# Optimization experiments

Hardware: AMD Instinct MI355X
Metric: run time of the kernel (lower is better)

The kernel has to match this reference:

```python
import jax, jax.numpy as jnp
import numpy as np

NEG = jnp.float32(-1e30)  # finite stand-in for -inf (grad-safe)
BLANK = 0


def setup_inputs() -> dict:
    key = jax.random.key(0)
    k1, k2, k3, k4 = jax.random.split(key, 4)
    B, T, V, S = 64, 1024, 128, 256
    logits = jax.random.normal(k1, (B, T, V), dtype=jnp.float32)
    log_probs = jax.nn.log_softmax(logits, axis=-1)  # valid log-probs like a model head
    log_probs_length = jax.random.randint(k2, (B,), 768, T + 1)
    text_encoded = jax.random.randint(k3, (B, S), 1, V)  # labels exclude blank=0
    text_encoded_length = jax.random.randint(k4, (B,), 64, S + 1)
    return {
        "log_probs": log_probs,
        "log_probs_length": log_probs_length,
        "text_encoded": text_encoded,
        "text_encoded_length": text_encoded_length,
    }


def _ctc_loss(log_probs, input_lengths, targets, target_lengths):
    """CTC loss, matching torch.nn.CTCLoss(blank=0, reduction='mean', zero_infinity=True)."""
    B, T, V = log_probs.shape
    S = targets.shape[1]
    L2 = 2 * S + 1  # extended label sequence: blank-interleaved

    # extended labels ext[b, s]: blank at even s, target[(s-1)//2] at odd s
    ext = jnp.full((B, L2), BLANK, dtype=targets.dtype)
    ext = ext.at[:, 1::2].set(targets)

    # gather per-step log-prob of each extended label: [B, T, L2]
    lp_ext = jnp.take_along_axis(
        log_probs, jnp.broadcast_to(ext[:, None, :], (B, T, L2)), axis=2
    )

    pos = jnp.arange(L2)
    valid_s = pos[None, :] < (2 * target_lengths[:, None] + 1)  # [B, L2]
    ext_m2 = jnp.pad(ext, ((0, 0), (2, 0)), constant_values=BLANK)[:, :-2]
    # skip transition s-2 -> s allowed only at non-blank (odd) positions with differing labels
    skip_mask = (pos[None, :] >= 2) & (pos[None, :] % 2 == 1) & (ext != ext_m2)

    alpha0 = jnp.full((B, L2), NEG, dtype=log_probs.dtype)
    alpha0 = alpha0.at[:, 0].set(lp_ext[:, 0, 0])
    alpha0 = alpha0.at[:, 1].set(jnp.where(target_lengths > 0, lp_ext[:, 0, 1], NEG))
    alpha0 = jnp.where(valid_s, alpha0, NEG)

    lp_ext_T = jnp.moveaxis(lp_ext, 1, 0)  # [T, B, L2]

    def step(alpha, x):
        lp_t, t = x
        s1 = jnp.pad(alpha, ((0, 0), (1, 0)), constant_values=NEG)[:, :-1]
        s2 = jnp.pad(alpha, ((0, 0), (2, 0)), constant_values=NEG)[:, :-2]
        a = jnp.logaddexp(alpha, s1)
        a = jnp.where(skip_mask, jnp.logaddexp(a, s2), a)
        new = jnp.where(valid_s, a + lp_t, NEG)
        # freeze alpha for samples whose input sequence has ended
        new = jnp.where((t < input_lengths)[:, None], new, alpha)
        return new, None

    alpha, _ = jax.lax.scan(step, alpha0, (lp_ext_T[1:], jnp.arange(1, T)))

    L = target_lengths
    idx1 = (2 * L)[:, None]
    idx0 = jnp.maximum(2 * L - 1, 0)[:, None]
    a_blank = jnp.take_along_axis(alpha, idx1, axis=1)[:, 0]
    a_label = jnp.take_along_axis(alpha, idx0, axis=1)[:, 0]
    ll = jnp.logaddexp(a_blank, jnp.where(L > 0, a_label, NEG))
    loss_b = -ll
    # zero_infinity: zero out infeasible alignments
    loss_b = jnp.where(loss_b > 1e29, jnp.float32(0.0), loss_b)
    # reduction='mean': divide each loss by its target length, then batch-mean
    return jnp.mean(loss_b / jnp.maximum(L, 1).astype(log_probs.dtype))


def reference(log_probs, log_probs_length, text_encoded, text_encoded_length):
    return _ctc_loss(log_probs, log_probs_length, text_encoded, text_encoded_length)
```

## Files before the change

kernel.cpp:

```cpp
#include <hip/hip_runtime.h>

constexpr int B_ = 64;
constexpr int T_ = 1024;
constexpr int V_ = 128;
constexpr int S_ = 256;
constexpr int GRING = 32;
constexpr int ROWF = 384;
constexpr int NGW = 3;
constexpr float INV_LN2 = 1.4426950408889634f;
constexpr float LN2 = 0.6931471805599453f;

#define WS_DUMPF(W, b) ((W) + 64 + (size_t)(b) * 640)
#define WS_DUMPB(W, b) ((W) + 64 + 64 * 640 + (size_t)(b) * 640)
#define WS_KARR(W)     ((int*)((W) + 64 + 2 * 64 * 640))

#define WG_SCOPE __HIP_MEMORY_SCOPE_WORKGROUP

template <int CTRL>
__device__ __forceinline__ float dpp_mov0(float x) {
    return __int_as_float(__builtin_amdgcn_update_dpp(
        0, __float_as_int(x), CTRL, 0xF, 0xF, false));
}
template <int CTRL>
__device__ __forceinline__ float dpp_max(float x) {
    const float s = __int_as_float(__builtin_amdgcn_update_dpp(
        __float_as_int(x), __float_as_int(x), CTRL, 0xF, 0xF, false));
    return fmaxf(x, s);
}

__device__ __forceinline__ void poll_eq(int* p, int want) {
    while (__hip_atomic_load(p, __ATOMIC_RELAXED, WG_SCOPE) != want)
        __builtin_amdgcn_s_sleep(1);
}

__device__ __forceinline__ int wave_rescale(float a[10], int& K) {
    float mx = a[0];
    #pragma unroll
    for (int k = 1; k < 10; ++k) mx = fmaxf(mx, a[k]);
    mx = dpp_max<0x111>(mx);
    mx = dpp_max<0x112>(mx);
    mx = dpp_max<0x114>(mx);
    mx = dpp_max<0x118>(mx);
    mx = dpp_max<0x142>(mx);
    mx = dpp_max<0x143>(mx);
    const float mall = __int_as_float(
        __builtin_amdgcn_readlane(__float_as_int(mx), 63));
    int e;
    (void)frexpf(mall, &e);
    const int ks = (mall > 0.0f) ? (124 - e) : 0;
    #pragma unroll
    for (int k = 0; k < 10; ++k) a[k] = ldexpf(a[k], ks);
    K += ks;
    return ks;
}

__global__ __launch_bounds__(256) void ctc_scan(
    const float* __restrict__ lp,
    const int* __restrict__ in_len,
    const int* __restrict__ tgt,
    const int* __restrict__ tgt_len,
    float* __restrict__ W)
{
    const int b    = blockIdx.x & 63;
    const int dir  = blockIdx.x >> 6;
    const int tid  = threadIdx.x;
    const int wid  = tid >> 6;
    const int lane = tid & 63;

    __shared__ float ring[GRING * ROWF];
    __shared__ int   tags[8];
    __shared__ int   cons;

    const int L  = tgt_len[b];
    const int Tb = in_len[b];
    const float* lpb = lp + (size_t)b * T_ * V_;
    const int* tg = tgt + b * S_;

    const int tm = (Tb - 2) >> 1;
    const int Uf = tm;
    const int Ub = Tb - 2 - tm;
    const int U  = dir ? Ub : Uf;

    if (tid == 0) cons = 0;
    if (tid < 8) tags[tid] = -1;
    __syncthreads();

    if (wid >= 1) {
        const int q = wid - 1;

        int   perm[5], oddc[5];
        float vmask[5];
        #pragma unroll
        for (int c = 0; c < 5; ++c) {
            const int j = 5 * lane + c;
            if (j < L) { const int lb = tg[j]; perm[c] = lb >> 1; oddc[c] = lb & 1; vmask[c] = 1.0f; }
            else       { perm[c] = 0; oddc[c] = 0; vmask[c] = 0.0f; }
        }

        float2 R0[4], R1[4];
        auto issue = [&](float2 (&Rb)[4], int m) {
            const int n = min(4, U - 4 * m);
            #pragma unroll
            for (int r = 0; r < 4; ++r) {
                if (r < n) {
                    const int u = 4 * m + 1 + r;
                    const int t = dir ? (Tb - 1 - u) : u;
                    Rb[r] = *(const float2*)(lpb + (size_t)t * V_ + 2 * lane);
                }
            }
        };
        auto process = [&](float2 (&Rb)[4], int m) {
            while (__hip_atomic_load(&cons, __ATOMIC_RELAXED, WG_SCOPE) < 4 * m - 28)
                __builtin_amdgcn_s_sleep(1);
            const int n = min(4, U - 4 * m);
            #pragma unroll
            for (int r = 0; r < 4; ++r) {
                if (r < n) {
                    const float e0 = __builtin_exp2f(Rb[r].x * INV_LN2);
                    const float e1 = __builtin_exp2f(Rb[r].y * INV_LN2);
                    const float b0 = __int_as_float(
                        __builtin_amdgcn_readfirstlane(__float_as_int(e0)));
                    float gv[5];
                    #pragma unroll
                    for (int c = 0; c < 5; ++c) {
                        const float lo = __shfl(e0, perm[c], 64);
                        const float hi = __shfl(e1, perm[c], 64);
                        gv[c] = vmask[c] * (oddc[c] ? hi : lo);
                    }
                    float* rb = ring + ((4 * m + r) & (GRING - 1)) * ROWF;
                    ((float2*)rb)[lane]         = make_float2(b0,    gv[0]);
                    ((float2*)(rb + 128))[lane] = make_float2(gv[1], gv[2]);
                    ((float2*)(rb + 256))[lane] = make_float2(gv[3], gv[4]);
                }
            }
            asm volatile("s_waitcnt lgkmcnt(0)" ::: "memory");
            if (lane == 0)
                __hip_atomic_store(&tags[m & 7], m, __ATOMIC_RELAXED, WG_SCOPE);
        };

        int m = q;
        if (4 * m + 1 <= U) {
            issue(R0, m);
            if (4 * (m + NGW) + 1 <= U) issue(R1, m + NGW);
            while (true) {
                process(R0, m);
                if (4 * (m + 2 * NGW) + 1 <= U) issue(R0, m + 2 * NGW);
                m += NGW;
                if (4 * m + 1 > U) break;
                process(R1, m);
                if (4 * (m + 2 * NGW) + 1 <= U) issue(R1, m + 2 * NGW);
                m += NGW;
                if (4 * m + 1 > U) break;
            }
        }
        return;
    }

    float2 S[4][12];
    auto readBlock = [&](int set, int m) {
        const int base = ((4 * m) & (GRING - 1)) * ROWF + 2 * lane;
        #pragma unroll
        for (int r = 0; r < 4; ++r)
            #pragma unroll
            for (int pl = 0; pl < 3; ++pl)
                S[set][r * 3 + pl] =
                    *(const float2*)&ring[base + r * ROWF + pl * 128];
    };

    if (dir == 0) {
        float skipf[5];
        #pragma unroll
        for (int c = 0; c < 5; ++c) {
            const int j = 5 * lane + c;
            skipf[c] = (j >= 1 && j < L && tg[j] != tg[j - 1]) ? 1.0f : 0.0f;
        }
        float a[10];
        #pragma unroll
        for (int k = 0; k < 10; ++k) a[k] = 0.0f;
        {
            const float p00 = __builtin_exp2f(lpb[0] * INV_LN2);
            const float p01 = __builtin_exp2f(lpb[tg[0]] * INV_LN2);
            if (lane == 0) { a[0] = p00; a[1] = p01; }
        }
        float u9n = 0.0f;
        int K = 0;

        auto rowCore = [&](float2 c0, float2 c1, float2 c2) {
            const float u9 = u9n;
            const float p0 = c0.x;
            a[9] = (a[9] + a[8] + skipf[4] * a[7]) * c2.y;
            u9n = dpp_mov0<0x138>(a[9]);
            a[8] = (a[8] + a[7]) * p0;
            a[7] = (a[7] + a[6] + skipf[3] * a[5]) * c2.x;
            a[6] = (a[6] + a[5]) * p0;
            a[5] = (a[5] + a[4] + skipf[2] * a[3]) * c1.y;
            a[4] = (a[4] + a[3]) * p0;
            a[3] = (a[3] + a[2] + skipf[1] * a[1]) * c1.x;
            a[2] = (a[2] + a[1]) * p0;
            a[1] = (a[1] + a[0] + skipf[0] * u9) * c0.y;
            a[0] = (a[0] + u9) * p0;
        };
        auto row4 = [&](int set) {
            #pragma unroll
            for (int r = 0; r < 4; ++r)
                rowCore(S[set][r * 3], S[set][r * 3 + 1], S[set][r * 3 + 2]);
        };
        auto body = [&](int m, int setc, int setp) {
            if (4 * (m + 2) + 1 <= Uf) {
                poll_eq(&tags[(m + 2) & 7], m + 2);
                readBlock(setp, m + 2);
            }
            row4(setc);
            if (lane == 0)
                __hip_atomic_store(&cons, 4 * m + 4, __ATOMIC_RELAXED, WG_SCOPE);
        };

        const int MB4 = (Uf / 4) & ~3;
        poll_eq(&tags[0], 0); readBlock(0, 0);
        poll_eq(&tags[1], 1); readBlock(1, 1);
        for (int mb = 0; mb < MB4; mb += 4) {
            body(mb + 0, 0, 2);
            body(mb + 1, 1, 3);
            { const int ks = wave_rescale(a, K); u9n = ldexpf(u9n, ks); }
            body(mb + 2, 2, 0);
            body(mb + 3, 3, 1);
            { const int ks = wave_rescale(a, K); u9n = ldexpf(u9n, ks); }
        }
        #pragma unroll
        for (int r = 0; r < 4; ++r)
            if (4 * MB4 + 1 + r <= Uf)
                rowCore(S[0][r * 3], S[0][r * 3 + 1], S[0][r * 3 + 2]);
        #pragma unroll
        for (int r = 0; r < 4; ++r)
            if (4 * MB4 + 5 + r <= Uf)
                rowCore(S[1][r * 3], S[1][r * 3 + 1], S[1][r * 3 + 2]);
        { const int ks = wave_rescale(a, K); u9n = ldexpf(u9n, ks); }
        for (int u = 4 * MB4 + 9; u <= Uf; ++u) {
            const int bu = (u - 1) >> 2;
            poll_eq(&tags[bu & 7], bu);
            const int base = ((u - 1) & (GRING - 1)) * ROWF + 2 * lane;
            const float2 c0 = *(const float2*)&ring[base];
            const float2 c1 = *(const float2*)&ring[base + 128];
            const float2 c2 = *(const float2*)&ring[base + 256];
            rowCore(c0, c1, c2);
        }

        float* dump = WS_DUMPF(W, b);
        #pragma unroll
        for (int k = 0; k < 10; ++k) dump[10 * lane + k] = a[k];
        if (lane == 0) WS_KARR(W)[b] = K;
    } else {
        float sB[5];
        #pragma unroll
        for (int c = 0; c < 5; ++c) {
            const int j = 5 * lane + c + 1;
            sB[c] = (j < L && tg[j] != tg[j - 1]) ? 1.0f : 0.0f;
        }
        float g[10];
        #pragma unroll
        for (int k = 0; k < 10; ++k) g[k] = 0.0f;
        {
            const float pb = __builtin_exp2f(lpb[(size_t)(Tb - 1) * V_] * INV_LN2);
            const float pl = __builtin_exp2f(lpb[(size_t)(Tb - 1) * V_ + tg[L - 1]] * INV_LN2);
            #pragma unroll
            for (int k = 0; k < 10; ++k) {
                const int s = 10 * lane + k;
                if (s == 2 * L)     g[k] = pb;
                if (s == 2 * L - 1) g[k] = pl;
            }
        }
        float d0n = dpp_mov0<0x130>(g[0]);
        float d1n = dpp_mov0<0x130>(g[1]);
        int K = 0;

        auto rowCore = [&](float2 c0, float2 c1, float2 c2) {
            const float d0 = d0n, d1 = d1n;
            const float p0 = c0.x;
            g[0] = (g[0] + g[1]) * p0;
            g[1] = (g[1] + g[2] + sB[0] * g[3]) * c0.y;
            d0n = dpp_mov0<0x130>(g[0]);
            d1n = dpp_mov0<0x130>(g[1]);
            g[2] = (g[2] + g[3]) * p0;
            g[3] = (g[3] + g[4] + sB[1] * g[5]) * c1.x;
            g[4] = (g[4] + g[5]) * p0;
            g[5] = (g[5] + g[6] + sB[2] * g[7]) * c1.y;
            g[6] = (g[6] + g[7]) * p0;
            g[7] = (g[7] + g[8] + sB[3] * g[9]) * c2.x;
            g[8] = (g[8] + g[9]) * p0;
            g[9] = (g[9] + d0 + sB[4] * d1) * c2.y;
        };
        auto row4 = [&](int set) {
            #pragma unroll
            for (int r = 0; r < 4; ++r)
                rowCore(S[set][r * 3], S[set][r * 3 + 1], S[set][r * 3 + 2]);
        };
        auto body = [&](int m, int setc, int setp) {
            if (4 * (m + 2) + 1 <= Ub) {
                poll_eq(&tags[(m + 2) & 7], m + 2);
                readBlock(setp, m + 2);
            }
            row4(setc);
            if (lane == 0)
                __hip_atomic_store(&cons, 4 * m + 4, __ATOMIC_RELAXED, WG_SCOPE);
        };

        const int MB4 = (Ub / 4) & ~3;
        poll_eq(&tags[0], 0); readBlock(0, 0);
        poll_eq(&tags[1], 1); readBlock(1, 1);
        for (int mb = 0; mb < MB4; mb += 4) {
            body(mb + 0, 0, 2);
            body(mb + 1, 1, 3);
            { const int ks = wave_rescale(g, K);
              d0n = ldexpf(d0n, ks); d1n = ldexpf(d1n, ks); }
            body(mb + 2, 2, 0);
            body(mb + 3, 3, 1);
            { const int ks = wave_rescale(g, K);
              d0n = ldexpf(d0n, ks); d1n = ldexpf(d1n, ks); }
        }
        #pragma unroll
        for (int r = 0; r < 4; ++r)
            if (4 * MB4 + 1 + r <= Ub)
                rowCore(S[0][r * 3], S[0][r * 3 + 1], S[0][r * 3 + 2]);
        #pragma unroll
        for (int r = 0; r < 4; ++r)
            if (4 * MB4 + 5 + r <= Ub)
                rowCore(S[1][r * 3], S[1][r * 3 + 1], S[1][r * 3 + 2]);
        { const int ks = wave_rescale(g, K);
          d0n = ldexpf(d0n, ks); d1n = ldexpf(d1n, ks); }
        for (int u = 4 * MB4 + 9; u <= Ub; ++u) {
            const int bu = (u - 1) >> 2;
            poll_eq(&tags[bu & 7], bu);
            const int base = ((u - 1) & (GRING - 1)) * ROWF + 2 * lane;
            const float2 c0 = *(const float2*)&ring[base];
            const float2 c1 = *(const float2*)&ring[base + 128];
            const float2 c2 = *(const float2*)&ring[base + 256];
            rowCore(c0, c1, c2);
        }

        {
            const float d0 = d0n, d1 = d1n;
            g[0] = g[0] + g[1];
            g[1] = g[1] + g[2] + sB[0] * g[3];
            g[2] = g[2] + g[3];
            g[3] = g[3] + g[4] + sB[1] * g[5];
            g[4] = g[4] + g[5];
            g[5] = g[5] + g[6] + sB[2] * g[7];
            g[6] = g[6] + g[7];
            g[7] = g[7] + g[8] + sB[3] * g[9];
            g[8] = g[8] + g[9];
            g[9] = g[9] + d0 + sB[4] * d1;
        }
        float* dump = WS_DUMPB(W, b);
        #pragma unroll
        for (int k = 0; k < 10; ++k) dump[10 * lane + k] = g[k];
        if (lane == 0) WS_KARR(W)[64 + b] = K;
    }
}

__global__ void ctc_join_kernel(const float* __restrict__ W_const,
                                const int* __restrict__ tgt_len,
                                float* __restrict__ lossArr) {
    const int b = blockIdx.x;
    const int lane = threadIdx.x;
    float* W = const_cast<float*>(W_const);
    const float* dA = WS_DUMPF(W, b);
    const float* dB = WS_DUMPB(W, b);
    double sum = 0.0;
    #pragma unroll
    for (int k = 0; k < 10; ++k)
        sum += (double)dA[10 * lane + k] * (double)dB[10 * lane + k];
    #pragma unroll
    for (int d = 1; d < 64; d <<= 1) sum += __shfl_xor(sum, d, 64);
    if (lane == 0) {
        const int L = tgt_len[b];
        const int KF = WS_KARR(W)[b];
        const int KB = WS_KARR(W)[64 + b];
        float loss = 0.0f;
        if (sum > 0.0) {
            const long long ub = __double_as_longlong(sum);
            const int ex = (int)((ub >> 52) & 2047) - 1023;
            const double f = __longlong_as_double(
                (ub & 0x000FFFFFFFFFFFFFLL) | 0x3FF0000000000000LL);
            const float ll2 = __builtin_log2f((float)f)
                            + (float)(ex - KF - KB);
            loss = -(ll2 * LN2);
            if (!(loss <= 1e29f)) loss = 0.0f;
        }
        lossArr[b] = loss / (float)L;
    }
}

__global__ void ctc_reduce_kernel(const float* __restrict__ ws, float* __restrict__ out) {
    float v = ws[threadIdx.x];
    #pragma unroll
    for (int o = 32; o > 0; o >>= 1) v += __shfl_down(v, o);
    if (threadIdx.x == 0) out[0] = v / (float)B_;
}

extern "C" void kernel_launch(void* const* d_in, const int* in_sizes, int n_in,
                              void* d_out, int out_size, void* d_ws, size_t ws_size,
                              hipStream_t stream) {
    const float* lp      = (const float*)d_in[0];
    const int*   in_len  = (const int*)d_in[1];
    const int*   tgt     = (const int*)d_in[2];
    const int*   tgt_len = (const int*)d_in[3];
    float* W   = (float*)d_ws;
    float* out = (float*)d_out;

    ctc_scan<<<2 * B_, 256, 0, stream>>>(lp, in_len, tgt, tgt_len, W);
    ctc_join_kernel<<<B_, 64, 0, stream>>>(W, tgt_len, W);
    ctc_reduce_kernel<<<1, 64, 0, stream>>>(W, out);
}
```

Baseline: 126.9 us.

## Replace producer-wave LDS ring with single-wave register-pipelined gather and scan

Drops the three producer waves, the shared-memory ring and the tag/consumer polling. A single 64-lane wave now loads rows of log-probs eight at a time into double-buffered registers, and does the exp and shuffle gather inline, one row ahead of the recurrence. This removes LDS traffic and spin-wait synchronisation from the serial critical path. In exchange, the exp and shuffle gather work now sits on the same wave as the dependent recurrence and can no longer run in parallel on other waves.

After: 187.4 us. 47.7% more time.

```diff
diff --git a/kernel.cpp b/kernel.cpp
--- a/kernel.cpp
+++ b/kernel.cpp
@@ -4,17 +4,12 @@
 constexpr int T_ = 1024;
 constexpr int V_ = 128;
 constexpr int S_ = 256;
-constexpr int GRING = 32;
-constexpr int ROWF = 384;
-constexpr int NGW = 3;
 constexpr float INV_LN2 = 1.4426950408889634f;
 constexpr float LN2 = 0.6931471805599453f;
 
 #define WS_DUMPF(W, b) ((W) + 64 + (size_t)(b) * 640)
 #define WS_DUMPB(W, b) ((W) + 64 + 64 * 640 + (size_t)(b) * 640)
 #define WS_KARR(W)     ((int*)((W) + 64 + 2 * 64 * 640))
-
-#define WG_SCOPE __HIP_MEMORY_SCOPE_WORKGROUP
 
 template <int CTRL>
 __device__ __forceinline__ float dpp_mov0(float x) {
@@ -26,11 +21,6 @@
     const float s = __int_as_float(__builtin_amdgcn_update_dpp(
         __float_as_int(x), __float_as_int(x), CTRL, 0xF, 0xF, false));
     return fmaxf(x, s);
-}
-
-__device__ __forceinline__ void poll_eq(int* p, int want) {
-    while (__hip_atomic_load(p, __ATOMIC_RELAXED, WG_SCOPE) != want)
-        __builtin_amdgcn_s_sleep(1);
 }
 
 __device__ __forceinline__ int wave_rescale(float a[10], int& K) {
@@ -54,7 +44,7 @@
     return ks;
 }
 
-__global__ __launch_bounds__(256) void ctc_scan(
+__global__ __launch_bounds__(64) void ctc_scan(
     const float* __restrict__ lp,
     const int* __restrict__ in_len,
     const int* __restrict__ tgt,
@@ -63,13 +53,7 @@
 {
     const int b    = blockIdx.x & 63;
     const int dir  = blockIdx.x >> 6;
-    const int tid  = threadIdx.x;
-    const int wid  = tid >> 6;
-    const int lane = tid & 63;
-
-    __shared__ float ring[GRING * ROWF];
-    __shared__ int   tags[8];
-    __shared__ int   cons;
+    const int lane = threadIdx.x;
 
     const int L  = tgt_len[b];
     const int Tb = in_len[b];
@@ -81,91 +65,44 @@
     const int Ub = Tb - 2 - tm;
     const int U  = dir ? Ub : Uf;
 
-    if (tid == 0) cons = 0;
-    if (tid < 8) tags[tid] = -1;
-    __syncthreads();
-
-    if (wid >= 1) {
-        const int q = wid - 1;
-
-        int   perm[5], oddc[5];
-        float vmask[5];
+    int   perm[5], oddc[5];
+    float vmask[5];
+    #pragma unroll
+    for (int c = 0; c < 5; ++c) {
+        const int j = 5 * lane + c;
+        if (j < L) { const int lb = tg[j]; perm[c] = lb >> 1; oddc[c] = lb & 1; vmask[c] = 1.0f; }
+        else       { perm[c] = 0; oddc[c] = 0; vmask[c] = 0.0f; }
+    }
+
+    auto loadRow = [&](int u) -> float2 {
+        const int t = dir ? (Tb - 1 - u) : u;
+        return *(const float2*)(lpb + (size_t)t * V_ + 2 * lane);
+    };
+    auto gather = [&](float2 Rv, float2& c0, float2& c1, float2& c2) {
+        const float e0 = __builtin_exp2f(Rv.x * INV_LN2);
+        const float e1 = __builtin_exp2f(Rv.y * INV_LN2);
+        const float p0 = __int_as_float(
+            __builtin_amdgcn_readfirstlane(__float_as_int(e0)));
+        float gv[5];
         #pragma unroll
         for (int c = 0; c < 5; ++c) {
-            const int j = 5 * lane + c;
-            if (j < L) { const int lb = tg[j]; perm[c] = lb >> 1; oddc[c] = lb & 1; vmask[c] = 1.0f; }
-            else       { perm[c] = 0; oddc[c] = 0; vmask[c] = 0.0f; }
-        }
-
-        float2 R0[4], R1[4];
-        auto issue = [&](float2 (&Rb)[4], int m) {
-            const int n = min(4, U - 4 * m);
-            #pragma unroll
-            for (int r = 0; r < 4; ++r) {
-                if (r < n) {
-                    const int u = 4 * m + 1 + r;
-                    const int t = dir ? (Tb - 1 - u) : u;
-                    Rb[r] = *(const float2*)(lpb + (size_t)t * V_ + 2 * lane);
-                }
-            }
-        };
-        auto process = [&](float2 (&Rb)[4], int m) {
-            while (__hip_atomic_load(&cons, __ATOMIC_RELAXED, WG_SCOPE) < 4 * m - 28)
-                __builtin_amdgcn_s_sleep(1);
-            const int n = min(4, U - 4 * m);
-            #pragma unroll
-            for (int r = 0; r < 4; ++r) {
-                if (r < n) {
-                    const float e0 = __builtin_exp2f(Rb[r].x * INV_LN2);
-                    const float e1 = __builtin_exp2f(Rb[r].y * INV_LN2);
-                    const float b0 = __int_as_float(
-                        __builtin_amdgcn_readfirstlane(__float_as_int(e0)));
-                    float gv[5];
-                    #pragma unroll
-                    for (int c = 0; c < 5; ++c) {
-                        const float lo = __shfl(e0, perm[c], 64);
-                        const float hi = __shfl(e1, perm[c], 64);
-                        gv[c] = vmask[c] * (oddc[c] ? hi : lo);
-                    }
-                    float* rb = ring + ((4 * m + r) & (GRING - 1)) * ROWF;
-                    ((float2*)rb)[lane]         = make_float2(b0,    gv[0]);
-                    ((float2*)(rb + 128))[lane] = make_float2(gv[1], gv[2]);
-                    ((float2*)(rb + 256))[lane] = make_float2(gv[3], gv[4]);
-                }
-            }
-            asm volatile("s_waitcnt lgkmcnt(0)" ::: "memory");
-            if (lane == 0)
-                __hip_atomic_store(&tags[m & 7], m, __ATOMIC_RELAXED, WG_SCOPE);
-        };
-
-        int m = q;
-        if (4 * m + 1 <= U) {
-            issue(R0, m);
-            if (4 * (m + NGW) + 1 <= U) issue(R1, m + NGW);
-            while (true) {
-                process(R0, m);
-                if (4 * (m + 2 * NGW) + 1 <= U) issue(R0, m + 2 * NGW);
-                m += NGW;
-                if (4 * m + 1 > U) break;
-                process(R1, m);
-                if (4 * (m + 2 * NGW) + 1 <= U) issue(R1, m + 2 * NGW);
-                m += NGW;
-                if (4 * m + 1 > U) break;
-            }
-        }
-        return;
-    }
-
-    float2 S[4][12];
-    auto readBlock = [&](int set, int m) {
-        const int base = ((4 * m) & (GRING - 1)) * ROWF + 2 * lane;
-        #pragma unroll
-        for (int r = 0; r < 4; ++r)
-            #pragma unroll
-            for (int pl = 0; pl < 3; ++pl)
-                S[set][r * 3 + pl] =
-                    *(const float2*)&ring[base + r * ROWF + pl * 128];
+            const float lo = __shfl(e0, perm[c], 64);
+            const float hi = __shfl(e1, perm[c], 64);
+            gv[c] = vmask[c] * (oddc[c] ? hi : lo);
+        }
+        c0 = make_float2(p0,    gv[0]);
+        c1 = make_float2(gv[1], gv[2]);
+        c2 = make_float2(gv[3], gv[4]);
     };
+
+    float2 RA[8], RB[8];
+    auto issueChunk = [&](float2 (&R)[8], int c) {
+        #pragma unroll
+        for (int r = 0; r < 8; ++r) R[r] = loadRow(8 * c + 1 + r);
+    };
+
+    const int nch   = U >> 3;
+    const int ntail = U & 7;
 
     if (dir == 0) {
         float skipf[5];
@@ -200,49 +137,37 @@
             a[1] = (a[1] + a[0] + skipf[0] * u9) * c0.y;
             a[0] = (a[0] + u9) * p0;
         };
-        auto row4 = [&](int set) {
-            #pragma unroll
-            for (int r = 0; r < 4; ++r)
-                rowCore(S[set][r * 3], S[set][r * 3 + 1], S[set][r * 3 + 2]);
+        auto processChunk = [&](float2 (&R)[8]) {
+            float2 c0, c1, c2, n0, n1, n2;
+            gather(R[0], c0, c1, c2);
+            #pragma unroll
+            for (int r = 0; r < 8; ++r) {
+                if (r < 7) gather(R[r + 1], n0, n1, n2);
+                rowCore(c0, c1, c2);
+                if (r < 7) { c0 = n0; c1 = n1; c2 = n2; }
+            }
+            const int ks = wave_rescale(a, K);
+            u9n = ldexpf(u9n, ks);
         };
-        auto body = [&](int m, int setc, int setp) {
-            if (4 * (m + 2) + 1 <= Uf) {
-                poll_eq(&tags[(m + 2) & 7], m + 2);
-                readBlock(setp, m + 2);
-            }
-            row4(setc);
-            if (lane == 0)
-                __hip_atomic_store(&cons, 4 * m + 4, __ATOMIC_RELAXED, WG_SCOPE);
-        };
-
-        const int MB4 = (Uf / 4) & ~3;
-        poll_eq(&tags[0], 0); readBlock(0, 0);
-        poll_eq(&tags[1], 1); readBlock(1, 1);
-        for (int mb = 0; mb < MB4; mb += 4) {
-            body(mb + 0, 0, 2);
-            body(mb + 1, 1, 3);
-            { const int ks = wave_rescale(a, K); u9n = ldexpf(u9n, ks); }
-            body(mb + 2, 2, 0);
-            body(mb + 3, 3, 1);
-            { const int ks = wave_rescale(a, K); u9n = ldexpf(u9n, ks); }
-        }
-        #pragma unroll
-        for (int r = 0; r < 4; ++r)
-            if (4 * MB4 + 1 + r <= Uf)
-                rowCore(S[0][r * 3], S[0][r * 3 + 1], S[0][r * 3 + 2]);
-        #pragma unroll
-        for (int r = 0; r < 4; ++r)
-            if (4 * MB4 + 5 + r <= Uf)
-                rowCore(S[1][r * 3], S[1][r * 3 + 1], S[1][r * 3 + 2]);
-        { const int ks = wave_rescale(a, K); u9n = ldexpf(u9n, ks); }
-        for (int u = 4 * MB4 + 9; u <= Uf; ++u) {
-            const int bu = (u - 1) >> 2;
-            poll_eq(&tags[bu & 7], bu);
-            const int base = ((u - 1) & (GRING - 1)) * ROWF + 2 * lane;
-            const float2 c0 = *(const float2*)&ring[base];
-            const float2 c1 = *(const float2*)&ring[base + 128];
-            const float2 c2 = *(const float2*)&ring[base + 256];
-            rowCore(c0, c1, c2);
+
+        issueChunk(RA, 0);
+        if (nch > 1) issueChunk(RB, 1);
+        for (int c = 0; c < nch; ++c) {
+            if ((c & 1) == 0) { processChunk(RA); if (c + 2 < nch) issueChunk(RA, c + 2); }
+            else              { processChunk(RB); if (c + 2 < nch) issueChunk(RB, c + 2); }
+        }
+        {
+            float2 RT[7];
+            #pragma unroll
+            for (int i = 0; i < 7; ++i)
+                if (i < ntail) RT[i] = loadRow(8 * nch + 1 + i);
+            #pragma unroll
+            for (int i = 0; i < 7; ++i)
+                if (i < ntail) {
+                    float2 c0, c1, c2;
+                    gather(RT[i], c0, c1, c2);
+                    rowCore(c0, c1, c2);
+                }
         }
 
         float* dump = WS_DUMPF(W, b);
@@ -289,52 +214,37 @@
             g[8] = (g[8] + g[9]) * p0;
             g[9] = (g[9] + d0 + sB[4] * d1) * c2.y;
         };
-        auto row4 = [&](int set) {
-            #pragma unroll
-            for (int r = 0; r < 4; ++r)
-                rowCore(S[set][r * 3], S[set][r * 3 + 1], S[set][r * 3 + 2]);
+        auto processChunk = [&](float2 (&R)[8]) {
+            float2 c0, c1, c2, n0, n1, n2;
+            gather(R[0], c0, c1, c2);
+            #pragma unroll
+            for (int r = 0; r < 8; ++r) {
+                if (r < 7) gather(R[r + 1], n0, n1, n2);
+                rowCore(c0, c1, c2);
+                if (r < 7) { c0 = n0; c1 = n1; c2 = n2; }
+            }
+            const int ks = wave_rescale(g, K);
+            d0n = ldexpf(d0n, ks); d1n = ldexpf(d1n, ks);
         };
-        auto body = [&](int m, int setc, int setp) {
-            if (4 * (m + 2) + 1 <= Ub) {
-                poll_eq(&tags[(m + 2) & 7], m + 2);
-                readBlock(setp, m + 2);
-            }
-            row4(setc);
-            if (lane == 0)
-                __hip_atomic_store(&cons, 4 * m + 4, __ATOMIC_RELAXED, WG_SCOPE);
-        };
-
-        const int MB4 = (Ub / 4) & ~3;
-        poll_eq(&tags[0], 0); readBlock(0, 0);
-        poll_eq(&tags[1], 1); readBlock(1, 1);
-        for (int mb = 0; mb < MB4; mb += 4) {
-            body(mb + 0, 0, 2);
-            body(mb + 1, 1, 3);
-            { const int ks = wave_rescale(g, K);
-              d0n = ldexpf(d0n, ks); d1n = ldexpf(d1n, ks); }
-            body(mb + 2, 2, 0);
-            body(mb + 3, 3, 1);
-            { const int ks = wave_rescale(g, K);
-              d0n = ldexpf(d0n, ks); d1n = ldexpf(d1n, ks); }
-        }
-        #pragma unroll
-        for (int r = 0; r < 4; ++r)
-            if (4 * MB4 + 1 + r <= Ub)
-                rowCore(S[0][r * 3], S[0][r * 3 + 1], S[0][r * 3 + 2]);
-        #pragma unroll
-        for (int r = 0; r < 4; ++r)
-            if (4 * MB4 + 5 + r <= Ub)
-                rowCore(S[1][r * 3], S[1][r * 3 + 1], S[1][r * 3 + 2]);
-        { const int ks = wave_rescale(g, K);
-          d0n = ldexpf(d0n, ks); d1n = ldexpf(d1n, ks); }
-        for (int u = 4 * MB4 + 9; u <= Ub; ++u) {
-            const int bu = (u - 1) >> 2;
-            poll_eq(&tags[bu & 7], bu);
-            const int base = ((u - 1) & (GRING - 1)) * ROWF + 2 * lane;
-            const float2 c0 = *(const float2*)&ring[base];
-            const float2 c1 = *(const float2*)&ring[base + 128];
-            const float2 c2 = *(const float2*)&ring[base + 256];
-            rowCore(c0, c1, c2);
+
+        issueChunk(RA, 0);
+        if (nch > 1) issueChunk(RB, 1);
+        for (int c = 0; c < nch; ++c) {
+            if ((c & 1) == 0) { processChunk(RA); if (c + 2 < nch) issueChunk(RA, c + 2); }
+            else              { processChunk(RB); if (c + 2 < nch) issueChunk(RB, c + 2); }
+        }
+        {
+            float2 RT[7];
+            #pragma unroll
+            for (int i = 0; i < 7; ++i)
+                if (i < ntail) RT[i] = loadRow(8 * nch + 1 + i);
+            #pragma unroll
+            for (int i = 0; i < 7; ++i)
+                if (i < ntail) {
+                    float2 c0, c1, c2;
+                    gather(RT[i], c0, c1, c2);
+                    rowCore(c0, c1, c2);
+                }
         }
 
         {
@@ -407,7 +317,7 @@
     float* W   = (float*)d_ws;
     float* out = (float*)d_out;
 
-    ctc_scan<<<2 * B_, 256, 0, stream>>>(lp, in_len, tgt, tgt_len, W);
+    ctc_scan<<<2 * B_, 64, 0, stream>>>(lp, in_len, tgt, tgt_len, W);
     ctc_join_kernel<<<B_, 64, 0, stream>>>(W, tgt_len, W);
     ctc_reduce_kernel<<<1, 64, 0, stream>>>(W, out);
 }
```

## Enlarge producer chunks to 16 rows, batch consumer reads, fuse join and reduce

Applied to the files above, without the earlier changes.

Producer waves now each prefetch and process 16 timesteps per chunk instead of 4. The LDS ring doubles to 64 rows and each row is repacked as a float4 plus a float2. The scan wave reads 8-row halves, rescales every 8 rows and publishes progress less often, cutting poll and sync overhead per step. The join and final-mean kernels are merged into one 256-thread launch to drop a kernel launch. In exchange the code uses more LDS and registers and adds more complex tail handling.

After: 143.7 us. +13.3%, slower.

```diff
diff --git a/kernel.cpp b/kernel.cpp
--- a/kernel.cpp
+++ b/kernel.cpp
@@ -4,8 +4,9 @@
 constexpr int T_ = 1024;
 constexpr int V_ = 128;
 constexpr int S_ = 256;
-constexpr int GRING = 32;
+constexpr int GRING = 64;
 constexpr int ROWF = 384;
+constexpr int NTAG = 4;
 constexpr int NGW = 3;
 constexpr float INV_LN2 = 1.4426950408889634f;
 constexpr float LN2 = 0.6931471805599453f;
@@ -15,6 +16,11 @@
 #define WS_KARR(W)     ((int*)((W) + 64 + 2 * 64 * 640))
 
 #define WG_SCOPE __HIP_MEMORY_SCOPE_WORKGROUP
+
+__device__ __forceinline__ void poll_eq(int* p, int want) {
+    while (__hip_atomic_load(p, __ATOMIC_RELAXED, WG_SCOPE) != want)
+        __builtin_amdgcn_s_sleep(1);
+}
 
 template <int CTRL>
 __device__ __forceinline__ float dpp_mov0(float x) {
@@ -26,11 +32,6 @@
     const float s = __int_as_float(__builtin_amdgcn_update_dpp(
         __float_as_int(x), __float_as_int(x), CTRL, 0xF, 0xF, false));
     return fmaxf(x, s);
-}
-
-__device__ __forceinline__ void poll_eq(int* p, int want) {
-    while (__hip_atomic_load(p, __ATOMIC_RELAXED, WG_SCOPE) != want)
-        __builtin_amdgcn_s_sleep(1);
 }
 
 __device__ __forceinline__ int wave_rescale(float a[10], int& K) {
@@ -68,7 +69,7 @@
     const int lane = tid & 63;
 
     __shared__ float ring[GRING * ROWF];
-    __shared__ int   tags[8];
+    __shared__ int   tags[NTAG];
     __shared__ int   cons;
 
     const int L  = tgt_len[b];
@@ -82,7 +83,7 @@
     const int U  = dir ? Ub : Uf;
 
     if (tid == 0) cons = 0;
-    if (tid < 8) tags[tid] = -1;
+    if (tid < NTAG) tags[tid] = -1;
     __syncthreads();
 
     if (wid >= 1) {
@@ -97,28 +98,27 @@
             else       { perm[c] = 0; oddc[c] = 0; vmask[c] = 0.0f; }
         }
 
-        float2 R0[4], R1[4];
-        auto issue = [&](float2 (&Rb)[4], int m) {
-            const int n = min(4, U - 4 * m);
-            #pragma unroll
-            for (int r = 0; r < 4; ++r) {
-                if (r < n) {
-                    const int u = 4 * m + 1 + r;
+        float2 R0[16], R1[16];
+        auto issue = [&](float2 (&R)[16], int h) {
+            #pragma unroll
+            for (int i = 0; i < 16; ++i) {
+                const int u = 16 * h + 1 + i;
+                if (u <= U) {
                     const int t = dir ? (Tb - 1 - u) : u;
-                    Rb[r] = *(const float2*)(lpb + (size_t)t * V_ + 2 * lane);
+                    R[i] = *(const float2*)(lpb + (size_t)t * V_ + 2 * lane);
                 }
             }
         };
-        auto process = [&](float2 (&Rb)[4], int m) {
-            while (__hip_atomic_load(&cons, __ATOMIC_RELAXED, WG_SCOPE) < 4 * m - 28)
+        auto process = [&](float2 (&R)[16], int h) {
+            while (__hip_atomic_load(&cons, __ATOMIC_RELAXED, WG_SCOPE) < 16 * h - 48)
                 __builtin_amdgcn_s_sleep(1);
-            const int n = min(4, U - 4 * m);
-            #pragma unroll
-            for (int r = 0; r < 4; ++r) {
-                if (r < n) {
-                    const float e0 = __builtin_exp2f(Rb[r].x * INV_LN2);
-                    const float e1 = __builtin_exp2f(Rb[r].y * INV_LN2);
-                    const float b0 = __int_as_float(
+            #pragma unroll
+            for (int i = 0; i < 16; ++i) {
+                const int u = 16 * h + 1 + i;
+                if (u <= U) {
+                    const float e0 = __builtin_exp2f(R[i].x * INV_LN2);
+                    const float e1 = __builtin_exp2f(R[i].y * INV_LN2);
+                    const float p0 = __int_as_float(
                         __builtin_amdgcn_readfirstlane(__float_as_int(e0)));
                     float gv[5];
                     #pragma unroll
@@ -127,45 +127,55 @@
                         const float hi = __shfl(e1, perm[c], 64);
                         gv[c] = vmask[c] * (oddc[c] ? hi : lo);
                     }
-                    float* rb = ring + ((4 * m + r) & (GRING - 1)) * ROWF;
-                    ((float2*)rb)[lane]         = make_float2(b0,    gv[0]);
-                    ((float2*)(rb + 128))[lane] = make_float2(gv[1], gv[2]);
-                    ((float2*)(rb + 256))[lane] = make_float2(gv[3], gv[4]);
+                    float* rb = ring + ((u - 1) & (GRING - 1)) * ROWF;
+                    *(float4*)&rb[4 * lane] = make_float4(p0, gv[0], gv[1], gv[2]);
+                    *(float2*)&rb[256 + 2 * lane] = make_float2(gv[3], gv[4]);
                 }
             }
             asm volatile("s_waitcnt lgkmcnt(0)" ::: "memory");
             if (lane == 0)
-                __hip_atomic_store(&tags[m & 7], m, __ATOMIC_RELAXED, WG_SCOPE);
+                __hip_atomic_store(&tags[h & (NTAG - 1)], h, __ATOMIC_RELAXED, WG_SCOPE);
         };
 
         int m = q;
-        if (4 * m + 1 <= U) {
+        if (16 * m + 1 <= U) {
             issue(R0, m);
-            if (4 * (m + NGW) + 1 <= U) issue(R1, m + NGW);
+            if (16 * (m + NGW) + 1 <= U) issue(R1, m + NGW);
             while (true) {
                 process(R0, m);
-                if (4 * (m + 2 * NGW) + 1 <= U) issue(R0, m + 2 * NGW);
+                if (16 * (m + 2 * NGW) + 1 <= U) issue(R0, m + 2 * NGW);
                 m += NGW;
-                if (4 * m + 1 > U) break;
+                if (16 * m + 1 > U) break;
                 process(R1, m);
-                if (4 * (m + 2 * NGW) + 1 <= U) issue(R1, m + 2 * NGW);
+                if (16 * (m + 2 * NGW) + 1 <= U) issue(R1, m + 2 * NGW);
                 m += NGW;
-                if (4 * m + 1 > U) break;
+                if (16 * m + 1 > U) break;
             }
         }
         return;
     }
 
-    float2 S[4][12];
-    auto readBlock = [&](int set, int m) {
-        const int base = ((4 * m) & (GRING - 1)) * ROWF + 2 * lane;
-        #pragma unroll
-        for (int r = 0; r < 4; ++r)
-            #pragma unroll
-            for (int pl = 0; pl < 3; ++pl)
-                S[set][r * 3 + pl] =
-                    *(const float2*)&ring[base + r * ROWF + pl * 128];
+    float4 A4[8], B4[8];
+    float2 A2[8], B2[8];
+    auto readHalfA = [&](int j) {
+        const int base = ((8 * j) & (GRING - 1)) * ROWF;
+        #pragma unroll
+        for (int r = 0; r < 8; ++r) {
+            A4[r] = *(const float4*)&ring[base + r * ROWF + 4 * lane];
+            A2[r] = *(const float2*)&ring[base + r * ROWF + 256 + 2 * lane];
+        }
     };
+    auto readHalfB = [&](int j) {
+        const int base = ((8 * j) & (GRING - 1)) * ROWF;
+        #pragma unroll
+        for (int r = 0; r < 8; ++r) {
+            B4[r] = *(const float4*)&ring[base + r * ROWF + 4 * lane];
+            B2[r] = *(const float2*)&ring[base + r * ROWF + 256 + 2 * lane];
+        }
+    };
+
+    const int NHfull = U >> 3;
+    const int lastH  = (U - 1) >> 3;
 
     if (dir == 0) {
         float skipf[5];
@@ -200,49 +210,57 @@
             a[1] = (a[1] + a[0] + skipf[0] * u9) * c0.y;
             a[0] = (a[0] + u9) * p0;
         };
-        auto row4 = [&](int set) {
-            #pragma unroll
-            for (int r = 0; r < 4; ++r)
-                rowCore(S[set][r * 3], S[set][r * 3 + 1], S[set][r * 3 + 2]);
-        };
-        auto body = [&](int m, int setc, int setp) {
-            if (4 * (m + 2) + 1 <= Uf) {
-                poll_eq(&tags[(m + 2) & 7], m + 2);
-                readBlock(setp, m + 2);
-            }
-            row4(setc);
+        auto consume8A = [&]() {
+            #pragma unroll
+            for (int r = 0; r < 8; ++r)
+                rowCore(make_float2(A4[r].x, A4[r].y),
+                        make_float2(A4[r].z, A4[r].w), A2[r]);
+        };
+        auto consume8B = [&]() {
+            #pragma unroll
+            for (int r = 0; r < 8; ++r)
+                rowCore(make_float2(B4[r].x, B4[r].y),
+                        make_float2(B4[r].z, B4[r].w), B2[r]);
+        };
+
+        poll_eq(&tags[0], 0);
+        readHalfA(0);
+        int j = 0;
+        while (j + 2 <= NHfull) {
+            { const int H = j + 1;
+              if (H <= lastH) {
+                  if ((H & 1) == 0) poll_eq(&tags[(H >> 1) & (NTAG - 1)], H >> 1);
+                  readHalfB(H);
+              } }
+            consume8A();
+            { const int ks = wave_rescale(a, K); u9n = ldexpf(u9n, ks); }
+            { const int H = j + 2;
+              if (H <= lastH) {
+                  if ((H & 1) == 0) poll_eq(&tags[(H >> 1) & (NTAG - 1)], H >> 1);
+                  readHalfA(H);
+              } }
+            consume8B();
+            { const int ks = wave_rescale(a, K); u9n = ldexpf(u9n, ks); }
             if (lane == 0)
-                __hip_atomic_store(&cons, 4 * m + 4, __ATOMIC_RELAXED, WG_SCOPE);
-        };
-
-        const int MB4 = (Uf / 4) & ~3;
-        poll_eq(&tags[0], 0); readBlock(0, 0);
-        poll_eq(&tags[1], 1); readBlock(1, 1);
-        for (int mb = 0; mb < MB4; mb += 4) {
-            body(mb + 0, 0, 2);
-            body(mb + 1, 1, 3);
+                __hip_atomic_store(&cons, 8 * (j + 2), __ATOMIC_RELAXED, WG_SCOPE);
+            j += 2;
+        }
+        if (j < NHfull) {
+            consume8A();
             { const int ks = wave_rescale(a, K); u9n = ldexpf(u9n, ks); }
-            body(mb + 2, 2, 0);
-            body(mb + 3, 3, 1);
-            { const int ks = wave_rescale(a, K); u9n = ldexpf(u9n, ks); }
-        }
-        #pragma unroll
-        for (int r = 0; r < 4; ++r)
-            if (4 * MB4 + 1 + r <= Uf)
-                rowCore(S[0][r * 3], S[0][r * 3 + 1], S[0][r * 3 + 2]);
-        #pragma unroll
-        for (int r = 0; r < 4; ++r)
-            if (4 * MB4 + 5 + r <= Uf)
-                rowCore(S[1][r * 3], S[1][r * 3 + 1], S[1][r * 3 + 2]);
-        { const int ks = wave_rescale(a, K); u9n = ldexpf(u9n, ks); }
-        for (int u = 4 * MB4 + 9; u <= Uf; ++u) {
-            const int bu = (u - 1) >> 2;
-            poll_eq(&tags[bu & 7], bu);
-            const int base = ((u - 1) & (GRING - 1)) * ROWF + 2 * lane;
-            const float2 c0 = *(const float2*)&ring[base];
-            const float2 c1 = *(const float2*)&ring[base + 128];
-            const float2 c2 = *(const float2*)&ring[base + 256];
-            rowCore(c0, c1, c2);
+            if (lane == 0)
+                __hip_atomic_store(&cons, 8 * (j + 1), __ATOMIC_RELAXED, WG_SCOPE);
+            j++;
+        }
+        if (8 * NHfull < U) {
+            const int sb = (8 * NHfull) >> 4;
+            poll_eq(&tags[sb & (NTAG - 1)], sb);
+            for (int u = 8 * NHfull + 1; u <= U; ++u) {
+                const int base = ((u - 1) & (GRING - 1)) * ROWF;
+                const float4 v4 = *(const float4*)&ring[base + 4 * lane];
+                const float2 v2 = *(const float2*)&ring[base + 256 + 2 * lane];
+                rowCore(make_float2(v4.x, v4.y), make_float2(v4.z, v4.w), v2);
+            }
         }
 
         float* dump = WS_DUMPF(W, b);
@@ -289,52 +307,60 @@
             g[8] = (g[8] + g[9]) * p0;
             g[9] = (g[9] + d0 + sB[4] * d1) * c2.y;
         };
-        auto row4 = [&](int set) {
-            #pragma unroll
-            for (int r = 0; r < 4; ++r)
-                rowCore(S[set][r * 3], S[set][r * 3 + 1], S[set][r * 3 + 2]);
-        };
-        auto body = [&](int m, int setc, int setp) {
-            if (4 * (m + 2) + 1 <= Ub) {
-                poll_eq(&tags[(m + 2) & 7], m + 2);
-                readBlock(setp, m + 2);
-            }
-            row4(setc);
-            if (lane == 0)
-                __hip_atomic_store(&cons, 4 * m + 4, __ATOMIC_RELAXED, WG_SCOPE);
-        };
-
-        const int MB4 = (Ub / 4) & ~3;
-        poll_eq(&tags[0], 0); readBlock(0, 0);
-        poll_eq(&tags[1], 1); readBlock(1, 1);
-        for (int mb = 0; mb < MB4; mb += 4) {
-            body(mb + 0, 0, 2);
-            body(mb + 1, 1, 3);
+        auto consume8A = [&]() {
+            #pragma unroll
+            for (int r = 0; r < 8; ++r)
+                rowCore(make_float2(A4[r].x, A4[r].y),
+                        make_float2(A4[r].z, A4[r].w), A2[r]);
+        };
+        auto consume8B = [&]() {
+            #pragma unroll
+            for (int r = 0; r < 8; ++r)
+                rowCore(make_float2(B4[r].x, B4[r].y),
+                        make_float2(B4[r].z, B4[r].w), B2[r]);
+        };
+
+        poll_eq(&tags[0], 0);
+        readHalfA(0);
+        int j = 0;
+        while (j + 2 <= NHfull) {
+            { const int H = j + 1;
+              if (H <= lastH) {
+                  if ((H & 1) == 0) poll_eq(&tags[(H >> 1) & (NTAG - 1)], H >> 1);
+                  readHalfB(H);
+              } }
+            consume8A();
             { const int ks = wave_rescale(g, K);
               d0n = ldexpf(d0n, ks); d1n = ldexpf(d1n, ks); }
-            body(mb + 2, 2, 0);
-            body(mb + 3, 3, 1);
+            { const int H = j + 2;
+              if (H <= lastH) {
+                  if ((H & 1) == 0) poll_eq(&tags[(H >> 1) & (NTAG - 1)], H >> 1);
+                  readHalfA(H);
+              } }
+            consume8B();
             { const int ks = wave_rescale(g, K);
               d0n = ldexpf(d0n, ks); d1n = ldexpf(d1n, ks); }
-        }
-        #pragma unroll
-        for (int r = 0; r < 4; ++r)
-            if (4 * MB4 + 1 + r <= Ub)
-                rowCore(S[0][r * 3], S[0][r * 3 + 1], S[0][r * 3 + 2]);
-        #pragma unroll
-        for (int r = 0; r < 4; ++r)
-            if (4 * MB4 + 5 + r <= Ub)
-                rowCore(S[1][r * 3], S[1][r * 3 + 1], S[1][r * 3 + 2]);
-        { const int ks = wave_rescale(g, K);
-          d0n = ldexpf(d0n, ks); d1n = ldexpf(d1n, ks); }
-        for (int u = 4 * MB4 + 9; u <= Ub; ++u) {
-            const int bu = (u - 1) >> 2;
-            poll_eq(&tags[bu & 7], bu);
-            const int base = ((u - 1) & (GRING - 1)) * ROWF + 2 * lane;
-            const float2 c0 = *(const float2*)&ring[base];
-            const float2 c1 = *(const float2*)&ring[base + 128];
-            const float2 c2 = *(const float2*)&ring[base + 256];
-            rowCore(c0, c1, c2);
+            if (lane == 0)
+                __hip_atomic_store(&cons, 8 * (j + 2), __ATOMIC_RELAXED, WG_SCOPE);
+            j += 2;
+        }
+        if (j < NHfull) {
+            consume8A();
+            { const int ks = wave_rescale(g, K);
+              d0n = ldexpf(d0n, ks); d1n = ldexpf(d1n, ks); }
+            if (lane == 0)
+                __hip_atomic_store(&cons, 8 * (j + 1), __ATOMIC_RELAXED, WG_SCOPE);
+            j++;
+        }
+        if (8 * NHfull < U) {
+            const int sb = (8 * NHfull) >> 4;
+            poll_eq(&tags[sb & (NTAG - 1)], sb);
+            for (int u = 8 * NHfull + 1; u <= U; ++u) {
+                const int base = ((u - 1) & (GRING - 1)) * ROWF;
+                const float4 v4 = *(const float4*)&ring[base + 4 * lane];
+                const float2 v2 = *(const float2*)&ring[base + 256 + 2 * lane];
+                rowCore(make_float2(v4.x, v4.y), make_float2(v4.z, v4.w), v2);
+            }
         }
 
         {
@@ -357,25 +383,27 @@
     }
 }
 
-__global__ void ctc_join_kernel(const float* __restrict__ W_const,
+__global__ void ctc_join_reduce(const float* __restrict__ W,
                                 const int* __restrict__ tgt_len,
-                                float* __restrict__ lossArr) {
-    const int b = blockIdx.x;
-    const int lane = threadIdx.x;
-    float* W = const_cast<float*>(W_const);
+                                float* __restrict__ out) {
+    const int tid = threadIdx.x;
+    const int b   = tid & 63;
+    const int q   = tid >> 6;
     const float* dA = WS_DUMPF(W, b);
     const float* dB = WS_DUMPB(W, b);
-    double sum = 0.0;
-    #pragma unroll
-    for (int k = 0; k < 10; ++k)
-        sum += (double)dA[10 * lane + k] * (double)dB[10 * lane + k];
-    #pragma unroll
-    for (int d = 1; d < 64; d <<= 1) sum += __shfl_xor(sum, d, 64);
-    if (lane == 0) {
-        const int L = tgt_len[b];
+    double part = 0.0;
+    #pragma unroll 4
+    for (int k = 160 * q; k < 160 * q + 160; ++k)
+        part += (double)dA[k] * (double)dB[k];
+    __shared__ double sh[256];
+    sh[tid] = part;
+    __syncthreads();
+    if (tid < 64) {
+        const double sum = sh[tid] + sh[tid + 64] + sh[tid + 128] + sh[tid + 192];
+        const int L  = tgt_len[b];
         const int KF = WS_KARR(W)[b];
         const int KB = WS_KARR(W)[64 + b];
-        float loss = 0.0f;
+        float lossv = 0.0f;
         if (sum > 0.0) {
             const long long ub = __double_as_longlong(sum);
             const int ex = (int)((ub >> 52) & 2047) - 1023;
@@ -383,18 +411,14 @@
                 (ub & 0x000FFFFFFFFFFFFFLL) | 0x3FF0000000000000LL);
             const float ll2 = __builtin_log2f((float)f)
                             + (float)(ex - KF - KB);
-            loss = -(ll2 * LN2);
-            if (!(loss <= 1e29f)) loss = 0.0f;
-        }
-        lossArr[b] = loss / (float)L;
+            lossv = -(ll2 * LN2);
+            if (!(lossv <= 1e29f)) lossv = 0.0f;
+        }
+        float v = lossv / (float)L;
+        #pragma unroll
+        for (int d = 1; d < 64; d <<= 1) v += __shfl_xor(v, d, 64);
+        if (tid == 0) out[0] = v / (float)B_;
     }
-}
-
-__global__ void ctc_reduce_kernel(const float* __restrict__ ws, float* __restrict__ out) {
-    float v = ws[threadIdx.x];
-    #pragma unroll
-    for (int o = 32; o > 0; o >>= 1) v += __shfl_down(v, o);
-    if (threadIdx.x == 0) out[0] = v / (float)B_;
 }
 
 extern "C" void kernel_launch(void* const* d_in, const int* in_sizes, int n_in,
@@ -408,6 +432,5 @@
     float* out = (float*)d_out;
 
     ctc_scan<<<2 * B_, 256, 0, stream>>>(lp, in_len, tgt, tgt_len, W);
-    ctc_join_kernel<<<B_, 64, 0, stream>>>(W, tgt_len, W);
-    ctc_reduce_kernel<<<1, 64, 0, stream>>>(W, out);
-}
+    ctc_join_reduce<<<1, 256, 0, stream>>>(W, tgt_len, out);
+}
```
